# Kernel optimization log

Hardware: AMD Instinct MI355X
Metric: run time of the kernel (lower is better)

The kernel has to match this reference:

```python
import jax, jax.numpy as jnp
import numpy as np

V, S, B, D, H, DH, FF = 98304, 1536, 2, 768, 24, 32, 3072
SCALE = 1.0 / float(np.sqrt(DH))  # 0.17677669529663687


def _ln(x, w, b, eps=1e-5):
    mu = jnp.mean(x, axis=-1, keepdims=True)
    var = jnp.mean(jnp.square(x - mu), axis=-1, keepdims=True)
    return (x - mu) * jax.lax.rsqrt(var + eps) * w + b


def _block(x, mask, ln1w, ln1b, wqkv, bqkv, wo, bo, ln2w, ln2b, wfc, bfc, wproj, bproj):
    # x: (S, B, D) Megatron layout; mask: (B, 1, S, S) bool, True = masked
    h = _ln(x, ln1w, ln1b)
    qkv = (h @ wqkv.T + bqkv).reshape(S, B, H, 3 * DH)  # interleaved q/k/v per head
    q, k, v = qkv[..., :DH], qkv[..., DH:2 * DH], qkv[..., 2 * DH:]
    q = jnp.transpose(q, (1, 2, 0, 3))  # (B, H, S, DH)
    k = jnp.transpose(k, (1, 2, 0, 3))
    v = jnp.transpose(v, (1, 2, 0, 3))
    scores = jnp.einsum('bhqd,bhkd->bhqk', q, k) * SCALE  # (B, H, S, S)
    scores = jnp.where(mask, jnp.float32(-10000.0), scores)
    p = jax.nn.softmax(scores, axis=-1)
    ctx = jnp.einsum('bhqk,bhkd->bhqd', p, v)
    ctx = jnp.transpose(ctx, (2, 0, 1, 3)).reshape(S, B, D)  # back to (S, B, D)
    x = x + ctx @ wo.T + bo  # attention residual (dropout treated as identity)
    h2 = _ln(x, ln2w, ln2b)
    m = jax.nn.gelu(h2 @ wfc.T + bfc, approximate=False)  # exact (erf) gelu as aten.gelu
    return x + m @ wproj.T + bproj


def _param_shapes():
    ps = [('wte', (V, D)), ('wpe', (S, D))]
    for l in ('l0', 'l1'):
        ps += [(l + '_ln1_w', (D,)), (l + '_ln1_b', (D,)),
               (l + '_wqkv', (3 * D, D)), (l + '_bqkv', (3 * D,)),
               (l + '_wo', (D, D)), (l + '_bo', (D,)),
               (l + '_ln2_w', (D,)), (l + '_ln2_b', (D,)),
               (l + '_wfc', (FF, D)), (l + '_bfc', (FF,)),
               (l + '_wproj', (D, FF)), (l + '_bproj', (D,))]
    ps += [('lnf_w', (D,)), ('lnf_b', (D,))]
    return ps


def setup_inputs() -> dict:
    key = jax.random.key(0)
    inp = {}
    inp['input_ids'] = jax.random.randint(jax.random.fold_in(key, 0), (B, S), 0, V, dtype=jnp.int32)
    inp['position_ids'] = jnp.broadcast_to(jnp.arange(S, dtype=jnp.int32), (B, S))
    causal = jnp.triu(jnp.ones((S, S), jnp.bool_), k=1)  # True above diagonal = masked
    inp['attn_mask'] = jnp.broadcast_to(causal, (B, 1, S, S))
    for i, (name, shape) in enumerate(_param_shapes()):
        k = jax.random.fold_in(key, 100 + i)
        if name in ('lnf_w',) or (('_ln' in name) and name.endswith('_w')):
            inp[name] = jnp.ones(shape, jnp.float32)
        else:
            inp[name] = jax.random.normal(k, shape, jnp.float32) * 0.02
    return inp


def reference(input_ids, position_ids, attn_mask,
              wte, wpe,
              l0_ln1_w, l0_ln1_b, l0_wqkv, l0_bqkv, l0_wo, l0_bo,
              l0_ln2_w, l0_ln2_b, l0_wfc, l0_bfc, l0_wproj, l0_bproj,
              l1_ln1_w, l1_ln1_b, l1_wqkv, l1_bqkv, l1_wo, l1_bo,
              l1_ln2_w, l1_ln2_b, l1_wfc, l1_bfc, l1_wproj, l1_bproj,
              lnf_w, lnf_b):
    x = wte[input_ids] + wpe[position_ids]  # (B, S, D)
    x = jnp.transpose(x, (1, 0, 2))  # (S, B, D)
    x = _block(x, attn_mask, l0_ln1_w, l0_ln1_b, l0_wqkv, l0_bqkv, l0_wo, l0_bo,
               l0_ln2_w, l0_ln2_b, l0_wfc, l0_bfc, l0_wproj, l0_bproj)
    x = _block(x, attn_mask, l1_ln1_w, l1_ln1_b, l1_wqkv, l1_bqkv, l1_wo, l1_bo,
               l1_ln2_w, l1_ln2_b, l1_wfc, l1_bfc, l1_wproj, l1_bproj)
    return _ln(x, lnf_w, lnf_b)  # (S, B, D)
```

## Files before the change

### kernel.cpp

```cpp
#include <hip/hip_runtime.h>
#include <cmath>
#include <type_traits>

typedef unsigned short u16;
typedef float  f32x4 __attribute__((ext_vector_type(4)));
typedef short  s16x8 __attribute__((ext_vector_type(8)));
typedef __bf16 b16x8 __attribute__((ext_vector_type(8)));

#define GLOBAL_AS __attribute__((address_space(1)))
#define LDS_AS    __attribute__((address_space(3)))

constexpr int S_  = 1536;
constexpr int B_  = 2;
constexpr int D_  = 768;
constexpr int H_  = 24;
constexpr int DH_ = 32;
constexpr int FF_ = 3072;
constexpr int N_  = S_ * B_;
constexpr int D3_ = 3 * D_;
constexpr float SCALE_ = 0.17677669529663687f;

template <typename T>
static __device__ inline auto mfma_try(T a, T b, f32x4 c, int)
    -> decltype(__builtin_amdgcn_mfma_f32_16x16x32_bf16(a, b, c, 0, 0, 0)) {
  return __builtin_amdgcn_mfma_f32_16x16x32_bf16(a, b, c, 0, 0, 0);
}
template <typename T>
static __device__ inline f32x4 mfma_try(T a, T b, f32x4 c, long) {
  b16x8 ab = __builtin_bit_cast(b16x8, a);
  b16x8 bb = __builtin_bit_cast(b16x8, b);
  return __builtin_amdgcn_mfma_f32_16x16x32_bf16(ab, bb, c, 0, 0, 0);
}
static __device__ inline f32x4 mfma_bf16(s16x8 a, s16x8 b, f32x4 c) {
  return mfma_try(a, b, c, 0);
}

static __device__ inline u16 f2bf(float f) {
  unsigned u = __builtin_bit_cast(unsigned, f);
  return (u16)((u + 0x7FFFu + ((u >> 16) & 1u)) >> 16);
}

static __device__ inline float rmax16(float v) {
  v = fmaxf(v, __shfl_xor(v, 1));
  v = fmaxf(v, __shfl_xor(v, 2));
  v = fmaxf(v, __shfl_xor(v, 4));
  v = fmaxf(v, __shfl_xor(v, 8));
  return v;
}
static __device__ inline float rsum16(float v) {
  v += __shfl_xor(v, 1);
  v += __shfl_xor(v, 2);
  v += __shfl_xor(v, 4);
  v += __shfl_xor(v, 8);
  return v;
}

__global__ void convert_weights_kernel(const float* __restrict__ wqkv,
                                       const float* __restrict__ wo,
                                       const float* __restrict__ wfc,
                                       const float* __restrict__ wproj,
                                       u16* __restrict__ dst) {
  constexpr int C0 = D3_ * D_;
  constexpr int C1 = C0 + D_ * D_;
  constexpr int C2 = C1 + FF_ * D_;
  constexpr int C3 = C2 + D_ * FF_;
  int i4 = (blockIdx.x * 256 + threadIdx.x) * 4;
  if (i4 >= C3) return;
  const float* src; int off;
  if (i4 < C0)      { src = wqkv;  off = i4; }
  else if (i4 < C1) { src = wo;    off = i4 - C0; }
  else if (i4 < C2) { src = wfc;   off = i4 - C1; }
  else              { src = wproj; off = i4 - C2; }
  float4 v = *(const float4*)(src + off);
  ushort4 o;
  o.x = f2bf(v.x); o.y = f2bf(v.y); o.z = f2bf(v.z); o.w = f2bf(v.w);
  *(ushort4*)(dst + i4) = o;
}

__global__ void embed_kernel(const int* __restrict__ ids, const int* __restrict__ pos,
                             const float* __restrict__ wte, const float* __restrict__ wpe,
                             float* __restrict__ x) {
  int g  = blockIdx.x * 256 + threadIdx.x;
  int i4 = g * 4;
  int row = i4 / D_;
  int d   = i4 - row * D_;
  int s = row >> 1, b = row & 1;
  int t = ids[b * S_ + s];
  int p = pos[b * S_ + s];
  float4 a = *(const float4*)(wte + (size_t)t * D_ + d);
  float4 c = *(const float4*)(wpe + (size_t)p * D_ + d);
  a.x += c.x; a.y += c.y; a.z += c.z; a.w += c.w;
  *(float4*)(x + i4) = a;
}

template <typename OUT>
__global__ void ln_kernel(const float* __restrict__ x, const float* __restrict__ w,
                          const float* __restrict__ b, OUT* __restrict__ out) {
  int wid = threadIdx.x >> 6, lane = threadIdx.x & 63;
  int tok = blockIdx.x * 4 + wid;
  const float* xr = x + (size_t)tok * D_;
  float4 v[3];
  float s = 0.f, ss = 0.f;
#pragma unroll
  for (int c = 0; c < 3; ++c) {
    v[c] = *(const float4*)(xr + c * 256 + lane * 4);
    s  += v[c].x + v[c].y + v[c].z + v[c].w;
    ss += v[c].x * v[c].x + v[c].y * v[c].y + v[c].z * v[c].z + v[c].w * v[c].w;
  }
#pragma unroll
  for (int m = 1; m <= 32; m <<= 1) { s += __shfl_xor(s, m); ss += __shfl_xor(ss, m); }
  float mu = s * (1.0f / D_);
  float var = ss * (1.0f / D_) - mu * mu;
  float rs = rsqrtf(var + 1e-5f);
#pragma unroll
  for (int c = 0; c < 3; ++c) {
    int d = c * 256 + lane * 4;
    float o0 = (v[c].x - mu) * rs * w[d + 0] + b[d + 0];
    float o1 = (v[c].y - mu) * rs * w[d + 1] + b[d + 1];
    float o2 = (v[c].z - mu) * rs * w[d + 2] + b[d + 2];
    float o3 = (v[c].w - mu) * rs * w[d + 3] + b[d + 3];
    if constexpr (std::is_same_v<OUT, u16>) {
      ushort4 o; o.x = f2bf(o0); o.y = f2bf(o1); o.z = f2bf(o2); o.w = f2bf(o3);
      *(ushort4*)(out + (size_t)tok * D_ + d) = o;
    } else {
      float4 o; o.x = o0; o.y = o1; o.z = o2; o.w = o3;
      *(float4*)(out + (size_t)tok * D_ + d) = o;
    }
  }
}

template <int BM, int BN, int EPI>
__launch_bounds__(256, 3)
__global__ void gemm_kernel(const u16* __restrict__ X, const u16* __restrict__ W,
                            const float* __restrict__ bias, int K,
                            u16* __restrict__ o0, u16* __restrict__ o1,
                            u16* __restrict__ o2, float* __restrict__ xio) {
  constexpr int BK = 64;
  constexpr int WM = BM / 2, WN = BN / 2, TM = WM / 16, TN = WN / 16;
  __shared__ u16 As[BM * BK];
  __shared__ u16 Bs[BN * BK];
  const int tid = threadIdx.x;
  const int wid = tid >> 6, lane = tid & 63;
  const int col = lane & 15, quad = lane >> 4;
  const int wm = wid & 1, wn = wid >> 1;
  const int rowA0 = blockIdx.x * BM;
  const int rowB0 = blockIdx.y * BN;

  f32x4 zz = {0.f, 0.f, 0.f, 0.f};
  f32x4 acc[TM][TN];
#pragma unroll
  for (int i = 0; i < TM; ++i)
#pragma unroll
    for (int j = 0; j < TN; ++j) acc[i][j] = zz;

  for (int k0 = 0; k0 < K; k0 += BK) {
#pragma unroll
    for (int it = 0; it < BM / 32; ++it) {
      int bs = (it * 4 + wid) * 64;
      int slot = bs + lane;
      int r = slot >> 3;
      int c = (slot & 7) ^ (r & 7);
      const u16* g = &X[(size_t)(rowA0 + r) * K + k0 + c * 8];
      __builtin_amdgcn_global_load_lds((const GLOBAL_AS unsigned int*)g,
                                       (LDS_AS unsigned int*)&As[bs * 8], 16, 0, 0);
    }
#pragma unroll
    for (int it = 0; it < BN / 32; ++it) {
      int bs = (it * 4 + wid) * 64;
      int slot = bs + lane;
      int r = slot >> 3;
      int c = (slot & 7) ^ (r & 7);
      const u16* g = &W[(size_t)(rowB0 + r) * K + k0 + c * 8];
      __builtin_amdgcn_global_load_lds((const GLOBAL_AS unsigned int*)g,
                                       (LDS_AS unsigned int*)&Bs[bs * 8], 16, 0, 0);
    }
    __syncthreads();
#pragma unroll
    for (int kb = 0; kb < 2; ++kb) {
      s16x8 af[TM], bf[TN];
#pragma unroll
      for (int ti = 0; ti < TM; ++ti) {
        int row = wm * WM + ti * 16 + col;
        af[ti] = *(const s16x8*)&As[row * BK + ((kb * 4 + quad) ^ (row & 7)) * 8];
      }
#pragma unroll
      for (int tj = 0; tj < TN; ++tj) {
        int row = wn * WN + tj * 16 + col;
        bf[tj] = *(const s16x8*)&Bs[row * BK + ((kb * 4 + quad) ^ (row & 7)) * 8];
      }
#pragma unroll
      for (int ti = 0; ti < TM; ++ti)
#pragma unroll
        for (int tj = 0; tj < TN; ++tj)
          acc[ti][tj] = mfma_bf16(af[ti], bf[tj], acc[ti][tj]);
    }
    __syncthreads();
  }

  const int tokBase  = rowA0 + wm * WM + quad * 4;
  const int featBase = rowB0 + wn * WN + col;
#pragma unroll
  for (int ti = 0; ti < TM; ++ti) {
#pragma unroll
    for (int tj = 0; tj < TN; ++tj) {
      int feat = featBase + tj * 16;
      float bv = bias[feat];
#pragma unroll
      for (int r = 0; r < 4; ++r) {
        int tok = tokBase + ti * 16 + r;
        float v = acc[ti][tj][r] + bv;
        if constexpr (EPI == 0) {
          int hh = feat / 96;
          int rem = feat - hh * 96;
          int comp = rem >> 5, d = rem & 31;
          int s = tok >> 1, bb = tok & 1;
          int bh = bb * H_ + hh;
          if (comp == 0)      o0[((size_t)bh * S_ + s) * DH_ + d] = f2bf(v);
          else if (comp == 1) o1[((size_t)bh * S_ + s) * DH_ + d] = f2bf(v);
          else                o2[((size_t)bh * DH_ + d) * S_ + s] = f2bf(v);
        } else if constexpr (EPI == 1) {
          float* p = xio + (size_t)tok * D_ + feat;
          *p = *p + v;
        } else {
          float g = 0.5f * v * (1.0f + erff(v * 0.70710678118654752f));
          o0[(size_t)tok * FF_ + feat] = f2bf(g);
        }
      }
    }
  }
}

__launch_bounds__(256)
__global__ void attn_kernel(const u16* __restrict__ q, const u16* __restrict__ k,
                            const u16* __restrict__ vt, u16* __restrict__ ctx) {
  __shared__ u16 Plds[4][16 * 40];
  const int tid = threadIdx.x;
  const int wid = tid >> 6, lane = tid & 63;
  const int col = lane & 15, quad = lane >> 4;
  const int bh = blockIdx.y;
  const int bb = bh / H_, hh = bh - bb * H_;
  const u16* qb = q  + (size_t)bh * S_ * DH_;
  const u16* kb = k  + (size_t)bh * S_ * DH_;
  const u16* vb = vt + (size_t)bh * DH_ * S_;
  const int q0 = blockIdx.x * 64 + wid * 16;

  s16x8 qf = *(const s16x8*)&qb[(q0 + col) * DH_ + quad * 8];
  f32x4 zz = {0.f, 0.f, 0.f, 0.f};
  f32x4 o0 = zz, o1 = zz;
  float mr[4] = {-1e30f, -1e30f, -1e30f, -1e30f};
  float lr[4] = {0.f, 0.f, 0.f, 0.f};

  const int kend = q0 + 16;
  for (int k0 = 0; k0 < kend; k0 += 32) {
    s16x8 kf0 = *(const s16x8*)&kb[(k0 + col) * DH_ + quad * 8];
    s16x8 kf1 = *(const s16x8*)&kb[(k0 + 16 + col) * DH_ + quad * 8];
    f32x4 s0 = mfma_bf16(qf, kf0, zz);
    f32x4 s1 = mfma_bf16(qf, kf1, zz);
#pragma unroll
    for (int r = 0; r < 4; ++r) {
      int qq = q0 + quad * 4 + r;
      float x0 = (k0 + col <= qq)      ? s0[r] * SCALE_ : -10000.0f;
      float x1 = (k0 + 16 + col <= qq) ? s1[r] * SCALE_ : -10000.0f;
      float cm = rmax16(fmaxf(x0, x1));
      float nm = fmaxf(mr[r], cm);
      float al = __expf(mr[r] - nm);
      float p0 = __expf(x0 - nm);
      float p1 = __expf(x1 - nm);
      float rs = rsum16(p0 + p1);
      lr[r] = lr[r] * al + rs;
      mr[r] = nm;
      o0[r] *= al; o1[r] *= al;
      Plds[wid][(quad * 4 + r) * 40 + col]      = f2bf(p0);
      Plds[wid][(quad * 4 + r) * 40 + 16 + col] = f2bf(p1);
    }
    __builtin_amdgcn_wave_barrier();
    __builtin_amdgcn_s_waitcnt(0xc07f);
    __builtin_amdgcn_wave_barrier();
    s16x8 pf  = *(const s16x8*)&Plds[wid][col * 40 + quad * 8];
    s16x8 vf0 = *(const s16x8*)&vb[(size_t)col * S_ + k0 + quad * 8];
    s16x8 vf1 = *(const s16x8*)&vb[(size_t)(16 + col) * S_ + k0 + quad * 8];
    o0 = mfma_bf16(pf, vf0, o0);
    o1 = mfma_bf16(pf, vf1, o1);
    __builtin_amdgcn_wave_barrier();
  }
#pragma unroll
  for (int r = 0; r < 4; ++r) {
    float inv = 1.0f / lr[r];
    int qq = q0 + quad * 4 + r;
    size_t base = ((size_t)qq * B_ + bb) * D_ + hh * DH_;
    ctx[base + col]      = f2bf(o0[r] * inv);
    ctx[base + 16 + col] = f2bf(o1[r] * inv);
  }
}

extern "C" void kernel_launch(void* const* d_in, const int* in_sizes, int n_in,
                              void* d_out, int out_size, void* d_ws, size_t ws_size,
                              hipStream_t stream) {
  const int*   ids = (const int*)d_in[0];
  const int*   pos = (const int*)d_in[1];
  const float* wte = (const float*)d_in[3];
  const float* wpe = (const float*)d_in[4];
  const float* lnf_w = (const float*)d_in[29];
  const float* lnf_b = (const float*)d_in[30];

  char* ws = (char*)d_ws;
  constexpr size_t SZ_X   = (size_t)N_ * D_ * 4;
  constexpr size_t SZ_H   = (size_t)N_ * D_ * 2;
  constexpr size_t SZ_QKV = (size_t)B_ * H_ * S_ * DH_ * 2;
  constexpr size_t SZ_M   = (size_t)N_ * FF_ * 2;
  constexpr int    WELEM  = D3_ * D_ + D_ * D_ + FF_ * D_ + D_ * FF_;

  float* xbuf = (float*)ws;
  u16* hbuf  = (u16*)(ws + SZ_X);
  u16* qbuf  = (u16*)(ws + SZ_X + SZ_H);
  u16* kbuf  = (u16*)(ws + SZ_X + SZ_H + SZ_QKV);
  u16* vtbuf = (u16*)(ws + SZ_X + SZ_H + 2 * SZ_QKV);
  u16* cbuf  = (u16*)(ws + SZ_X + SZ_H + 3 * SZ_QKV);
  u16* mbuf  = (u16*)(ws + SZ_X + SZ_H + 4 * SZ_QKV);
  u16* wbf   = (u16*)(ws + SZ_X + SZ_H + 4 * SZ_QKV + SZ_M);

  embed_kernel<<<N_ * D_ / 4 / 256, 256, 0, stream>>>(ids, pos, wte, wpe, xbuf);

  for (int l = 0; l < 2; ++l) {
    int p = 5 + l * 12;
    const float* ln1w  = (const float*)d_in[p + 0];
    const float* ln1b  = (const float*)d_in[p + 1];
    const float* wqkv  = (const float*)d_in[p + 2];
    const float* bqkv  = (const float*)d_in[p + 3];
    const float* wo    = (const float*)d_in[p + 4];
    const float* bo    = (const float*)d_in[p + 5];
    const float* ln2w  = (const float*)d_in[p + 6];
    const float* ln2b  = (const float*)d_in[p + 7];
    const float* wfc   = (const float*)d_in[p + 8];
    const float* bfc   = (const float*)d_in[p + 9];
    const float* wproj = (const float*)d_in[p + 10];
    const float* bproj = (const float*)d_in[p + 11];

    u16* wb = wbf + (size_t)l * WELEM;
    u16* wqkv_b  = wb;
    u16* wo_b    = wb + D3_ * D_;
    u16* wfc_b   = wb + D3_ * D_ + D_ * D_;
    u16* wproj_b = wb + D3_ * D_ + D_ * D_ + FF_ * D_;

    convert_weights_kernel<<<WELEM / 4 / 256, 256, 0, stream>>>(wqkv, wo, wfc, wproj, wb);

    ln_kernel<u16><<<N_ / 4, 256, 0, stream>>>(xbuf, ln1w, ln1b, hbuf);
    gemm_kernel<128, 128, 0><<<dim3(N_ / 128, D3_ / 128), 256, 0, stream>>>(
        hbuf, wqkv_b, bqkv, D_, qbuf, kbuf, vtbuf, nullptr);
    attn_kernel<<<dim3(S_ / 64, B_ * H_), 256, 0, stream>>>(qbuf, kbuf, vtbuf, cbuf);
    gemm_kernel<128, 64, 1><<<dim3(N_ / 128, D_ / 64), 256, 0, stream>>>(
        cbuf, wo_b, bo, D_, nullptr, nullptr, nullptr, xbuf);
    ln_kernel<u16><<<N_ / 4, 256, 0, stream>>>(xbuf, ln2w, ln2b, hbuf);
    gemm_kernel<128, 128, 2><<<dim3(N_ / 128, FF_ / 128), 256, 0, stream>>>(
        hbuf, wfc_b, bfc, D_, mbuf, nullptr, nullptr, nullptr);
    gemm_kernel<128, 64, 1><<<dim3(N_ / 128, D_ / 64), 256, 0, stream>>>(
        mbuf, wproj_b, bproj, FF_, nullptr, nullptr, nullptr, xbuf);
  }

  ln_kernel<float><<<N_ / 4, 256, 0, stream>>>(xbuf, lnf_w, lnf_b, (float*)d_out);
}
```

Before: 840.0 us.

## Double-buffer GEMM LDS tiles, split-K residual GEMMs with atomics, shrink tiles

Double-buffers the A/B LDS tiles so the next K-slice loads while MFMAs run on the current one, using explicit vmcnt waits and raw barriers in place of __syncthreads. Adds split-K across gridDim.z for the out-projection and FC2 GEMMs, which now accumulate into the fp32 residual with atomicAdd, and only slice zero adds the bias. Shrinks the QKV and FC1 tiles to 64x128 to launch more blocks. This targets load latency and low occupancy on the small residual GEMMs, at the cost of doubled LDS, atomic traffic and nondeterministic summation order.

```diff
diff --git a/kernel.cpp b/kernel.cpp
--- a/kernel.cpp
+++ b/kernel.cpp
@@ -137,14 +137,18 @@
                             u16* __restrict__ o2, float* __restrict__ xio) {
   constexpr int BK = 64;
   constexpr int WM = BM / 2, WN = BN / 2, TM = WM / 16, TN = WN / 16;
-  __shared__ u16 As[BM * BK];
-  __shared__ u16 Bs[BN * BK];
+  constexpr unsigned WAIT_NV = 0x0F70u | (unsigned)(BM / 32 + BN / 32);
+  __shared__ u16 As[2][BM * BK];
+  __shared__ u16 Bs[2][BN * BK];
   const int tid = threadIdx.x;
   const int wid = tid >> 6, lane = tid & 63;
   const int col = lane & 15, quad = lane >> 4;
   const int wm = wid & 1, wn = wid >> 1;
   const int rowA0 = blockIdx.x * BM;
   const int rowB0 = blockIdx.y * BN;
+  const int ksl    = K / (int)gridDim.z;
+  const int kstart = (int)blockIdx.z * ksl;
+  const int nIter  = ksl / BK;
 
   f32x4 zz = {0.f, 0.f, 0.f, 0.f};
   f32x4 acc[TM][TN];
@@ -153,16 +157,16 @@
 #pragma unroll
     for (int j = 0; j < TN; ++j) acc[i][j] = zz;
 
-  for (int k0 = 0; k0 < K; k0 += BK) {
+  auto stage = [&](int d, int kglob) {
 #pragma unroll
     for (int it = 0; it < BM / 32; ++it) {
       int bs = (it * 4 + wid) * 64;
       int slot = bs + lane;
       int r = slot >> 3;
       int c = (slot & 7) ^ (r & 7);
-      const u16* g = &X[(size_t)(rowA0 + r) * K + k0 + c * 8];
-      __builtin_amdgcn_global_load_lds((const GLOBAL_AS unsigned int*)g,
-                                       (LDS_AS unsigned int*)&As[bs * 8], 16, 0, 0);
+      __builtin_amdgcn_global_load_lds(
+          (const GLOBAL_AS unsigned int*)&X[(size_t)(rowA0 + r) * K + kglob + c * 8],
+          (LDS_AS unsigned int*)&As[d][bs * 8], 16, 0, 0);
     }
 #pragma unroll
     for (int it = 0; it < BN / 32; ++it) {
@@ -170,23 +174,36 @@
       int slot = bs + lane;
       int r = slot >> 3;
       int c = (slot & 7) ^ (r & 7);
-      const u16* g = &W[(size_t)(rowB0 + r) * K + k0 + c * 8];
-      __builtin_amdgcn_global_load_lds((const GLOBAL_AS unsigned int*)g,
-                                       (LDS_AS unsigned int*)&Bs[bs * 8], 16, 0, 0);
-    }
-    __syncthreads();
+      __builtin_amdgcn_global_load_lds(
+          (const GLOBAL_AS unsigned int*)&W[(size_t)(rowB0 + r) * K + kglob + c * 8],
+          (LDS_AS unsigned int*)&Bs[d][bs * 8], 16, 0, 0);
+    }
+  };
+
+  stage(0, kstart);
+  for (int i = 0; i < nIter; ++i) {
+    if (i + 1 < nIter) {
+      stage((i + 1) & 1, kstart + (i + 1) * BK);
+      __builtin_amdgcn_s_waitcnt(WAIT_NV);
+    } else {
+      __builtin_amdgcn_s_waitcnt(0x0F70u);
+    }
+    __builtin_amdgcn_s_barrier();
+    __builtin_amdgcn_sched_barrier(0);
+    const u16* Ab = As[i & 1];
+    const u16* Bb = Bs[i & 1];
 #pragma unroll
     for (int kb = 0; kb < 2; ++kb) {
       s16x8 af[TM], bf[TN];
 #pragma unroll
       for (int ti = 0; ti < TM; ++ti) {
         int row = wm * WM + ti * 16 + col;
-        af[ti] = *(const s16x8*)&As[row * BK + ((kb * 4 + quad) ^ (row & 7)) * 8];
+        af[ti] = *(const s16x8*)&Ab[row * BK + ((kb * 4 + quad) ^ (row & 7)) * 8];
       }
 #pragma unroll
       for (int tj = 0; tj < TN; ++tj) {
         int row = wn * WN + tj * 16 + col;
-        bf[tj] = *(const s16x8*)&Bs[row * BK + ((kb * 4 + quad) ^ (row & 7)) * 8];
+        bf[tj] = *(const s16x8*)&Bb[row * BK + ((kb * 4 + quad) ^ (row & 7)) * 8];
       }
 #pragma unroll
       for (int ti = 0; ti < TM; ++ti)
@@ -194,17 +211,19 @@
         for (int tj = 0; tj < TN; ++tj)
           acc[ti][tj] = mfma_bf16(af[ti], bf[tj], acc[ti][tj]);
     }
-    __syncthreads();
+    __builtin_amdgcn_sched_barrier(0);
+    __builtin_amdgcn_s_barrier();
   }
 
   const int tokBase  = rowA0 + wm * WM + quad * 4;
   const int featBase = rowB0 + wn * WN + col;
+  const bool addb = (blockIdx.z == 0);
 #pragma unroll
   for (int ti = 0; ti < TM; ++ti) {
 #pragma unroll
     for (int tj = 0; tj < TN; ++tj) {
       int feat = featBase + tj * 16;
-      float bv = bias[feat];
+      float bv = addb ? bias[feat] : 0.f;
 #pragma unroll
       for (int r = 0; r < 4; ++r) {
         int tok = tokBase + ti * 16 + r;
@@ -219,8 +238,7 @@
           else if (comp == 1) o1[((size_t)bh * S_ + s) * DH_ + d] = f2bf(v);
           else                o2[((size_t)bh * DH_ + d) * S_ + s] = f2bf(v);
         } else if constexpr (EPI == 1) {
-          float* p = xio + (size_t)tok * D_ + feat;
-          *p = *p + v;
+          atomicAdd(xio + (size_t)tok * D_ + feat, v);
         } else {
           float g = 0.5f * v * (1.0f + erff(v * 0.70710678118654752f));
           o0[(size_t)tok * FF_ + feat] = f2bf(g);
@@ -345,15 +363,15 @@
     convert_weights_kernel<<<WELEM / 4 / 256, 256, 0, stream>>>(wqkv, wo, wfc, wproj, wb);
 
     ln_kernel<u16><<<N_ / 4, 256, 0, stream>>>(xbuf, ln1w, ln1b, hbuf);
-    gemm_kernel<128, 128, 0><<<dim3(N_ / 128, D3_ / 128), 256, 0, stream>>>(
+    gemm_kernel<64, 128, 0><<<dim3(N_ / 64, D3_ / 128), 256, 0, stream>>>(
         hbuf, wqkv_b, bqkv, D_, qbuf, kbuf, vtbuf, nullptr);
     attn_kernel<<<dim3(S_ / 64, B_ * H_), 256, 0, stream>>>(qbuf, kbuf, vtbuf, cbuf);
-    gemm_kernel<128, 64, 1><<<dim3(N_ / 128, D_ / 64), 256, 0, stream>>>(
+    gemm_kernel<128, 64, 1><<<dim3(N_ / 128, D_ / 64, 2), 256, 0, stream>>>(
         cbuf, wo_b, bo, D_, nullptr, nullptr, nullptr, xbuf);
     ln_kernel<u16><<<N_ / 4, 256, 0, stream>>>(xbuf, ln2w, ln2b, hbuf);
-    gemm_kernel<128, 128, 2><<<dim3(N_ / 128, FF_ / 128), 256, 0, stream>>>(
+    gemm_kernel<64, 128, 2><<<dim3(N_ / 64, FF_ / 128), 256, 0, stream>>>(
         hbuf, wfc_b, bfc, D_, mbuf, nullptr, nullptr, nullptr);
-    gemm_kernel<128, 64, 1><<<dim3(N_ / 128, D_ / 64), 256, 0, stream>>>(
+    gemm_kernel<128, 64, 1><<<dim3(N_ / 128, D_ / 64, 2), 256, 0, stream>>>(
         mbuf, wproj_b, bproj, FF_, nullptr, nullptr, nullptr, xbuf);
   }
 
```

Measured after the change: 852.6 us. Within noise of the previous version (+1.5%).
